# Kernel optimization log

Hardware: AMD Instinct MI355X
Metric: run time of the kernel (lower is better)

Reference implementation:

```python
import jax, jax.numpy as jnp
import numpy as np

S, T, B, IN, H, O = 64, 32, 512, 66, 1024, 1024  # S == max_length


def _gru_cell(x, h, Wih, Whh, bih, bhh):
    # PyTorch GRU cell: gates ordered (r, z, n)
    gi = x @ Wih.T + bih            # [B, 3H]
    gh = h @ Whh.T + bhh            # [B, 3H]
    ir, iz, inn = jnp.split(gi, 3, axis=1)
    hr, hz, hn = jnp.split(gh, 3, axis=1)
    r = jax.nn.sigmoid(ir + hr)
    z = jax.nn.sigmoid(iz + hz)
    n = jnp.tanh(inn + r * hn)
    return (1.0 - z) * n + z * h


def setup_inputs() -> dict:
    key = jax.random.key(0)
    ks = jax.random.split(key, 20)
    s = 0.02
    return {
        "input_tensor": jax.random.normal(ks[0], (S, B, IN), jnp.float32),
        "target_tensor": jax.random.normal(ks[1], (T, B, H), jnp.float32),
        # encoder GRU
        "enc_Wih": jax.random.normal(ks[2], (3 * H, IN), jnp.float32) * s,
        "enc_Whh": jax.random.normal(ks[3], (3 * H, H), jnp.float32) * s,
        "enc_bih": jax.random.normal(ks[4], (3 * H,), jnp.float32) * s,
        "enc_bhh": jax.random.normal(ks[5], (3 * H,), jnp.float32) * s,
        # attention: Linear(2H -> max_length)
        "attn_W": jax.random.normal(ks[6], (S, 2 * H), jnp.float32) * s,
        "attn_b": jax.random.normal(ks[7], (S,), jnp.float32) * s,
        # attn_combine: Linear(2H -> H)
        "comb_W": jax.random.normal(ks[8], (H, 2 * H), jnp.float32) * s,
        "comb_b": jax.random.normal(ks[9], (H,), jnp.float32) * s,
        # decoder GRU
        "dec_Wih": jax.random.normal(ks[10], (3 * H, H), jnp.float32) * s,
        "dec_Whh": jax.random.normal(ks[11], (3 * H, H), jnp.float32) * s,
        "dec_bih": jax.random.normal(ks[12], (3 * H,), jnp.float32) * s,
        "dec_bhh": jax.random.normal(ks[13], (3 * H,), jnp.float32) * s,
        # output: Linear(H -> O)
        "out_W": jax.random.normal(ks[14], (O, H), jnp.float32) * s,
        "out_b": jax.random.normal(ks[15], (O,), jnp.float32) * s,
    }


def reference(input_tensor, target_tensor, enc_Wih, enc_Whh, enc_bih, enc_bhh,
              attn_W, attn_b, comb_W, comb_b, dec_Wih, dec_Whh, dec_bih,
              dec_bhh, out_W, out_b):
    batch = input_tensor.shape[1]
    h0 = jnp.zeros((batch, enc_Whh.shape[1]), input_tensor.dtype)

    # ---- encoder GRU over time ----
    def enc_step(h, x):
        h2 = _gru_cell(x, h, enc_Wih, enc_Whh, enc_bih, enc_bhh)
        return h2, h2

    enc_h, enc_out = jax.lax.scan(enc_step, h0, input_tensor)  # enc_out: [S, B, H]

    # ---- attention decoder, teacher forcing; loop t = 1..T-1 uses target[t-1] ----
    def dec_step(h, x):
        aw = jax.nn.softmax(jnp.concatenate([x, h], axis=1) @ attn_W.T + attn_b,
                            axis=1)                              # [B, S]
        ctx = jnp.einsum('bl,lbh->bh', aw, enc_out)              # [B, H]
        comb = jax.nn.relu(jnp.concatenate([x, ctx], axis=1) @ comb_W.T + comb_b)
        h2 = _gru_cell(comb, h, dec_Wih, dec_Whh, dec_bih, dec_bhh)
        out = jax.nn.log_softmax(h2 @ out_W.T + out_b, axis=1)   # [B, O]
        return h2, out

    _, outs = jax.lax.scan(dec_step, enc_h, target_tensor[:-1])
    # original overwrites `outputs` every step -> only last step survives
    return outs[-1]
```

## Files before the change

### kernel.cpp

```cpp
#include <hip/hip_runtime.h>
#include <hip/hip_bf16.h>
#include <math.h>

#define S_LEN 64
#define T_LEN 32
#define BATCH 512
#define IN_DIM 66
#define INP 128
#define H_DIM 1024
#define O_DIM 1024
#define H3 3072

typedef __attribute__((ext_vector_type(8))) short short8;
typedef __attribute__((ext_vector_type(4))) float f32x4;
typedef __attribute__((ext_vector_type(4))) unsigned short us4;

__device__ __forceinline__ unsigned short f2b(float f) {
    union { float f; unsigned u; } x; x.f = f;
    unsigned r = x.u + 0x7FFF + ((x.u >> 16) & 1);
    return (unsigned short)(r >> 16);
}
__device__ __forceinline__ float b2f(unsigned short s) {
    union { unsigned u; float f; } x; x.u = ((unsigned)s) << 16;
    return x.f;
}
__device__ __forceinline__ void gll16(const void* g, const void* l) {
    __builtin_amdgcn_global_load_lds(
        (const __attribute__((address_space(1))) unsigned int*)g,
        (__attribute__((address_space(3))) unsigned int*)l, 16, 0, 0);
}

template<int TM, int TN>
__global__ __launch_bounds__(256) void gemm_k(
    const unsigned short* __restrict__ A, int lda,
    const unsigned short* __restrict__ W, int ldw,
    const float* __restrict__ bias,
    const float* __restrict__ addf, const unsigned short* __restrict__ addb,
    int ldadd,
    float* __restrict__ Cf,
    unsigned short* __restrict__ Cb, int ldc,
    int K, int flags)
{
    constexpr int IF = TM / 16;
    constexpr int JF = TN / 64;
    constexpr int NW = TN / 4;
    constexpr int CA = TM * 4;
    constexpr int CW = TN * 4;
    __shared__ __align__(16) unsigned short As[2][TM * 32];
    __shared__ __align__(16) unsigned short Bs[2][TN * 32];

    const int bm = blockIdx.y * TM;
    const int bn = blockIdx.x * TN;
    const int t = threadIdx.x;
    const int lane = t & 63;
    const int wv = t >> 6;
    const int ln = lane & 15;
    const int quad = lane >> 4;

    f32x4 acc[IF][JF];
    #pragma unroll
    for (int i = 0; i < IF; i++)
        #pragma unroll
// ... 41 lines not shown
            af[ii] = *(const short8*)&As[cur][(ii * 16 + ln) * 32 + quad * 8];
        #pragma unroll
        for (int j = 0; j < JF; j++)
            bf[j] = *(const short8*)&Bs[cur][(wv * NW + j * 16 + ln) * 32 + quad * 8];
        #pragma unroll
        for (int ii = 0; ii < IF; ii++)
            #pragma unroll
            for (int j = 0; j < JF; j++)
                acc[ii][j] = __builtin_amdgcn_mfma_f32_16x16x32_bf16(
                    af[ii], bf[j], acc[ii][j], 0, 0, 0);
        __syncthreads();
    }

    #pragma unroll
    for (int i = 0; i < IF; i++) {
        #pragma unroll
        for (int j = 0; j < JF; j++) {
            #pragma unroll
            for (int r = 0; r < 4; r++) {
                int m = bm + i * 16 + quad * 4 + r;
                int n = bn + wv * NW + j * 16 + ln;
                float v = acc[i][j][r];
                if (flags & 1) v += bias[n];
                if (flags & 2) v += addf[(size_t)m * ldadd + n];
                if (flags & 4) v += b2f(addb[(size_t)m * ldadd + n]);
                if (flags & 8) v = fmaxf(v, 0.f);
                if (flags & 16) Cf[(size_t)m * ldc + n] = v;
                if (flags & 32) Cb[(size_t)m * ldc + n] = f2b(v);
            }
        }
    }
}

__device__ __forceinline__ void gru_stage(
    const unsigned short* __restrict__ A, int lda,
    const unsigned short* __restrict__ W, int ldw, int kb,
    unsigned short* As_g, unsigned short* Ws_g,
    int bm, int bn, int gt, int gwv)
{
    {
        int s = gt >> 7, r = (gt >> 2) & 31, c = gt & 3;
        gll16(A + (size_t)(bm + r) * lda + kb + s * 32 + c * 8,
              (const char*)As_g + gwv * 1024);
    }
    #pragma unroll
    for (int j = 0; j < 6; j++) {
        int ch = j * 256 + gt;
        int g2 = ch >> 9, ch2 = ch & 511;
        int s = ch2 >> 8, r = (ch2 >> 2) & 63, c = ch2 & 3;
        gll16(W + (size_t)(g2 * H_DIM + bn + r) * ldw + kb + s * 32 + c * 8,
              (const char*)Ws_g + j * 4096 + gwv * 1024);
    }
}

__device__ __forceinline__ void gru_compute(
    const unsigned short* As_g, const unsigned short* Ws_g,
    int gwv, int ln, int quad,
    f32x4 (&accR)[2], f32x4 (&accZ)[2], f32x4 (&accN)[2])
{
    #pragma unroll
    for (int sub = 0; sub < 2; sub++) {
        short8 a[2], bw[3];
        #pragma unroll
        for (int i = 0; i < 2; i++)
            a[i] = *(const short8*)&As_g[sub * 1024 + (i * 16 + ln) * 32 + quad * 8];
        #pragma unroll
        for (int g = 0; g < 3; g++)
            bw[g] = *(const short8*)&Ws_g[g * 4096 + sub * 2048 + (gwv * 16 + ln) * 32 + quad * 8];
        #pragma unroll
        for (int i = 0; i < 2; i++) {
            accR[i] = __builtin_amdgcn_mfma_f32_16x16x32_bf16(a[i], bw[0], accR[i], 0, 0, 0);
            accZ[i] = __builtin_amdgcn_mfma_f32_16x16x32_bf16(a[i], bw[1], accZ[i], 0, 0, 0);
            accN[i] = __builtin_amdgcn_mfma_f32_16x16x32_bf16(a[i], bw[2], accN[i], 0, 0, 0);
        }
    }
}

__global__ __launch_bounds__(512) void gru_gemm(
    const unsigned short* __restrict__ A0, int lda0,
    const unsigned short* __restrict__ W0, int ldw0, int K0,
    const unsigned short* __restrict__ A1,
    const unsigned short* __restrict__ W1,
    const float* __restrict__ bih, const float* __restrict__ bhh,
    const float* __restrict__ hf_in, float* __restrict__ hf_out,
    unsigned short* __restrict__ hb_out, unsigned short* __restrict__ slot)
{
    __shared__ __align__(16) unsigned short As2[2][2][2 * 32 * 32];
    __shared__ __align__(16) unsigned short Ws2[2][2][3 * 2 * 64 * 32];
    const int bm = blockIdx.y * 32;
    const int bn = blockIdx.x * 64;
    const int t = threadIdx.x;
    const int wg = t >> 8;
    const int gt = t & 255;
    const int lane = t & 63;
    const int gwv = gt >> 6;
    const int ln = lane & 15;
    const int quad = lane >> 4;

    f32x4 accR[2], accZ[2], accN0[2], accN1[2];
    #pragma unroll
    for (int i = 0; i < 2; i++) {
        f32x4 z = {0.f, 0.f, 0.f, 0.f};
        accR[i] = z; accZ[i] = z; accN0[i] = z; accN1[i] = z;
    }

    const int half0 = K0 >> 1;
    const int nt0 = half0 >> 6;
    const int nt = nt0 + 8;

    auto stg = [&](int i, int buf) {
        const unsigned short* A; int lda; const unsigned short* W; int ldw; int kb;
        if (i < nt0) { A = A0; lda = lda0; W = W0; ldw = ldw0; kb = wg * half0 + (i << 6); }
        else         { A = A1; lda = H_DIM; W = W1; ldw = H_DIM; kb = wg * 512 + ((i - nt0) << 6); }
        gru_stage(A, lda, W, ldw, kb, As2[wg][buf], Ws2[wg][buf], bm, bn, gt, gwv);
    };

    stg(0, 0);
    __syncthreads();
    for (int i = 0; i < nt; ++i) {
        const int cur = i & 1;
        if (i + 1 < nt) stg(i + 1, cur ^ 1);
        if (i < nt0)
            gru_compute(As2[wg][cur], Ws2[wg][cur], gwv, ln, quad, accR, accZ, accN0);
        else
            gru_compute(As2[wg][cur], Ws2[wg][cur], gwv, ln, quad, accR, accZ, accN1);
        __syncthreads();
    }

    float* red = (float*)Ws2;
    const int rb = (gwv * 64 + lane) * 33;
    if (wg == 1) {
        #pragma unroll
        for (int i = 0; i < 2; i++)
            #pragma unroll
            for (int r = 0; r < 4; r++) {
                red[rb + i * 4 + r]      = accR[i][r];
                red[rb + 8 + i * 4 + r]  = accZ[i][r];
                red[rb + 16 + i * 4 + r] = accN0[i][r];
                red[rb + 24 + i * 4 + r] = accN1[i][r];
            }
    }
    __syncthreads();
    if (wg == 0) {
        #pragma unroll
        for (int i = 0; i < 2; i++)
            #pragma unroll
            for (int r = 0; r < 4; r++) {
                accR[i][r]  += red[rb + i * 4 + r];
                accZ[i][r]  += red[rb + 8 + i * 4 + r];
                accN0[i][r] += red[rb + 16 + i * 4 + r];
                accN1[i][r] += red[rb + 24 + i * 4 + r];
            }
        const int n = bn + gwv * 16 + ln;
        const float br = bih[n] + bhh[n];
        const float bz = bih[H_DIM + n] + bhh[H_DIM + n];
        const float bi_n = bih[2 * H_DIM + n];
        const float bh_n = bhh[2 * H_DIM + n];
        #pragma unroll
        for (int i = 0; i < 2; i++) {
            #pragma unroll
            for (int r = 0; r < 4; r++) {
                const int m = bm + i * 16 + quad * 4 + r;
                const size_t idx = (size_t)m * H_DIM + n;
                float rg = 1.f / (1.f + __expf(-(accR[i][r] + br)));
                float zg = 1.f / (1.f + __expf(-(accZ[i][r] + bz)));
                float av = accN0[i][r] + bi_n + rg * (accN1[i][r] + bh_n);
                float e2 = __expf(-2.f * fabsf(av));
                float th = (1.f - e2) / (1.f + e2);
                th = av < 0.f ? -th : th;
                float o = (1.f - zg) * th + zg * hf_in[idx];
                hf_out[idx] = o;
                unsigned short ob = f2b(o);
                hb_out[idx] = ob;
                if (slot) slot[idx] = ob;
            }
        }
    }
}

__global__ __launch_bounds__(256) void attn_ctx(
    const unsigned short* __restrict__ hb,
    const unsigned short* __restrict__ wAhT,
    const unsigned short* __restrict__ attnx_t,
    const unsigned short* __restrict__ encb,
    unsigned short* __restrict__ ctx)
{
    __shared__ float hf[H_DIM];
    __shared__ float part[4][S_LEN];
    __shared__ float awl[S_LEN];
    const int b = blockIdx.x, t = threadIdx.x;
    {
        us4 u = *(const us4*)(hb + ((size_t)b << 10) + t * 4);
        #pragma unroll
        for (int j = 0; j < 4; j++) hf[t * 4 + j] = b2f(u[j]);
    }
    __syncthreads();
    {
        const int c = t & 63, ks = (t >> 6) * 256;
        float s = 0.f;
        #pragma unroll 8
        for (int k = 0; k < 256; k++)
            s += hf[ks + k] * b2f(wAhT[(size_t)(ks + k) * S_LEN + c]);
        part[t >> 6][c] = s;
    }
    __syncthreads();
    if (t < 64) {
        float v = part[0][t] + part[1][t] + part[2][t] + part[3][t]
                + b2f(attnx_t[b * S_LEN + t]);
        float m = v;
        #pragma unroll
        for (int off = 32; off; off >>= 1) m = fmaxf(m, __shfl_xor(m, off));
        float e = __expf(v - m);
        float ss = e;
        #pragma unroll
        for (int off = 32; off; off >>= 1) ss += __shfl_xor(ss, off);
        awl[t] = e / ss;
    }
    __syncthreads();
    const int hq = t * 4;
    float s0 = 0.f, s1 = 0.f, s2 = 0.f, s3 = 0.f;
    #pragma unroll 4
    for (int l = 0; l < S_LEN; l++) {
        us4 u = *(const us4*)(encb + (((size_t)l * BATCH + b) << 10) + hq);
        float w = awl[l];
        s0 += w * b2f(u[0]); s1 += w * b2f(u[1]);
        s2 += w * b2f(u[2]); s3 += w * b2f(u[3]);
    }
    us4 o; o[0] = f2b(s0); o[1] = f2b(s1); o[2] = f2b(s2); o[3] = f2b(s3);
    *(us4*)(ctx + ((size_t)b << 10) + hq) = o;
}

__global__ void cvt_w4(const float* __restrict__ src, int ld,
                       unsigned short* __restrict__ dst, int rows, int cols)
{
    int idx = blockIdx.x * blockDim.x + threadIdx.x;
    int total4 = rows * cols / 4;
    if (idx >= total4) return;
    int e = idx * 4;
    int r = e / cols, c = e - r * cols;
    const float* s = src + (size_t)r * ld + c;
    us4 o;
    #pragma unroll
    for (int j = 0; j < 4; j++) o[j] = f2b(s[j]);
    *(us4*)(dst + e) = o;
}

__global__ void cvt_plain4(const float* __restrict__ src,
                           unsigned short* __restrict__ dst, int total4)
{
    int idx = blockIdx.x * blockDim.x + threadIdx.x;
    if (idx >= total4) return;
    f32x4 v = *(const f32x4*)(src + (size_t)idx * 4);
    us4 o;
    #pragma unroll
    for (int j = 0; j < 4; j++) o[j] = f2b(v[j]);
    *(us4*)(dst + (size_t)idx * 4) = o;
}

__global__ void cvt_pad(const float* __restrict__ src, int scols,
                        unsigned short* __restrict__ dst, int dcols, int total)
{
    int idx = blockIdx.x * blockDim.x + threadIdx.x;
    if (idx >= total) return;
    int r = idx / dcols, c = idx - r * dcols;
    dst[idx] = (c < scols) ? f2b(src[(size_t)r * scols + c]) : (unsigned short)0;
}

__global__ void cvt_attT(const float* __restrict__ attn_W,
                         unsigned short* __restrict__ dst)
{
    int idx = blockIdx.x * blockDim.x + threadIdx.x;
    if (idx >= S_LEN * H_DIM) return;
    int k = idx >> 6, c = idx & 63;
    dst[idx] = f2b(attn_W[(size_t)c * 2 * H_DIM + H_DIM + k]);
}

__global__ void log_softmax1024(float* __restrict__ x)
{
    __shared__ float red[256];
    float* xr = x + (size_t)blockIdx.x * O_DIM;
    int t = threadIdx.x;
    float m = -1e30f;
    for (int i = t; i < O_DIM; i += 256) m = fmaxf(m, xr[i]);
    red[t] = m; __syncthreads();
    for (int s2 = 128; s2 > 0; s2 >>= 1) {
        if (t < s2) red[t] = fmaxf(red[t], red[t + s2]);
        __syncthreads();
    }
    m = red[0];
    __syncthreads();
    float s = 0.f;
    for (int i = t; i < O_DIM; i += 256) s += expf(xr[i] - m);
    red[t] = s; __syncthreads();
    for (int s2 = 128; s2 > 0; s2 >>= 1) {
        if (t < s2) red[t] += red[t + s2];
        __syncthreads();
    }
    float lse = m + logf(red[0]);
    __syncthreads();
    for (int i = t; i < O_DIM; i += 256) xr[i] = xr[i] - lse;
}

extern "C" void kernel_launch(void* const* d_in, const int* in_sizes, int n_in,
                              void* d_out, int out_size, void* d_ws, size_t ws_size,
                              hipStream_t stream)
{
    const float* input   = (const float*)d_in[0];
// ... 6 lines not shown
    const float* attn_b  = (const float*)d_in[7];
    const float* comb_W  = (const float*)d_in[8];
    const float* comb_b  = (const float*)d_in[9];
    const float* dec_Wih = (const float*)d_in[10];
    const float* dec_Whh = (const float*)d_in[11];
    const float* dec_bih = (const float*)d_in[12];
    const float* dec_bhh = (const float*)d_in[13];
    const float* out_W   = (const float*)d_in[14];
    const float* out_b   = (const float*)d_in[15];
    float* out = (float*)d_out;

    char* p = (char*)d_ws;
    auto alloc = [&](size_t bytes) {
        char* r = p; p += (bytes + 255) & ~(size_t)255; return r;
    };
    unsigned short* wWhh  = (unsigned short*)alloc((size_t)H3 * H_DIM * 2);
    unsigned short* wDih  = (unsigned short*)alloc((size_t)H3 * H_DIM * 2);
    unsigned short* wDhh  = (unsigned short*)alloc((size_t)H3 * H_DIM * 2);
    unsigned short* wCc   = (unsigned short*)alloc((size_t)H_DIM * H_DIM * 2);
    unsigned short* wCx   = (unsigned short*)alloc((size_t)H_DIM * H_DIM * 2);
    unsigned short* wO    = (unsigned short*)alloc((size_t)O_DIM * H_DIM * 2);
    unsigned short* wAhT  = (unsigned short*)alloc((size_t)H_DIM * S_LEN * 2);
    unsigned short* wAx   = (unsigned short*)alloc((size_t)S_LEN * H_DIM * 2);
    unsigned short* wIhp  = (unsigned short*)alloc((size_t)H3 * INP * 2);
    unsigned short* xbp   = (unsigned short*)alloc((size_t)S_LEN * BATCH * INP * 2);
    unsigned short* encb  = (unsigned short*)alloc((size_t)S_LEN * BATCH * H_DIM * 2);
    unsigned short* combx = (unsigned short*)alloc((size_t)(T_LEN - 1) * BATCH * H_DIM * 2);
    unsigned short* attnx = (unsigned short*)alloc((size_t)(T_LEN - 1) * BATCH * S_LEN * 2);
    float*          h     = (float*)alloc((size_t)BATCH * H_DIM * 4);
    unsigned short* hbA   = (unsigned short*)alloc((size_t)BATCH * H_DIM * 2);
    unsigned short* hbB   = (unsigned short*)alloc((size_t)BATCH * H_DIM * 2);
    unsigned short* ctx   = (unsigned short*)alloc((size_t)BATCH * H_DIM * 2);
    unsigned short* comb  = (unsigned short*)alloc((size_t)BATCH * H_DIM * 2);
    unsigned short* targetb = encb;

    const dim3 blk(256);

    hipMemsetAsync(h,   0, (size_t)BATCH * H_DIM * 4, stream);
    hipMemsetAsync(hbA, 0, (size_t)BATCH * H_DIM * 2, stream);

    cvt_w4<<<(H3 * H_DIM / 4 + 255) / 256, blk, 0, stream>>>(enc_Whh, H_DIM, wWhh, H3, H_DIM);
    cvt_w4<<<(H3 * H_DIM / 4 + 255) / 256, blk, 0, stream>>>(dec_Wih, H_DIM, wDih, H3, H_DIM);
    cvt_w4<<<(H3 * H_DIM / 4 + 255) / 256, blk, 0, stream>>>(dec_Whh, H_DIM, wDhh, H3, H_DIM);
    cvt_w4<<<(H_DIM * H_DIM / 4 + 255) / 256, blk, 0, stream>>>(comb_W + H_DIM, 2 * H_DIM, wCc, H_DIM, H_DIM);
    cvt_w4<<<(H_DIM * H_DIM / 4 + 255) / 256, blk, 0, stream>>>(comb_W, 2 * H_DIM, wCx, H_DIM, H_DIM);
    cvt_w4<<<(O_DIM * H_DIM / 4 + 255) / 256, blk, 0, stream>>>(out_W, H_DIM, wO, O_DIM, H_DIM);
    cvt_w4<<<(S_LEN * H_DIM / 4 + 255) / 256, blk, 0, stream>>>(attn_W, 2 * H_DIM, wAx, S_LEN, H_DIM);
    cvt_attT<<<(S_LEN * H_DIM + 255) / 256, blk, 0, stream>>>(attn_W, wAhT);
    cvt_pad<<<((S_LEN * BATCH * INP) + 255) / 256, blk, 0, stream>>>(
        input, IN_DIM, xbp, INP, S_LEN * BATCH * INP);
    cvt_pad<<<((H3 * INP) + 255) / 256, blk, 0, stream>>>(
        enc_Wih, IN_DIM, wIhp, INP, H3 * INP);
    cvt_plain4<<<((T_LEN * BATCH * H_DIM / 4) + 255) / 256, blk, 0, stream>>>(
        target, targetb, T_LEN * BATCH * H_DIM / 4);

    const int MT = (T_LEN - 1) * BATCH;
    gemm_k<64, 64><<<dim3(1, MT / 64), blk, 0, stream>>>(
        targetb, H_DIM, wAx, H_DIM, attn_b,
        nullptr, nullptr, 0, nullptr, attnx, S_LEN, H_DIM, 1 | 32);
    gemm_k<128, 128><<<dim3(H_DIM / 128, MT / 128), blk, 0, stream>>>(
        targetb, H_DIM, wCx, H_DIM, comb_b,
        nullptr, nullptr, 0, nullptr, combx, H_DIM, H_DIM, 1 | 32);

    const dim3 grid_gru(H_DIM / 64, BATCH / 32);
    const dim3 blk512(512);
    unsigned short* hcur = hbA;
    unsigned short* hnxt = hbB;

    for (int s = 0; s < S_LEN; s++) {
        gru_gemm<<<grid_gru, blk512, 0, stream>>>(
            xbp + (size_t)s * BATCH * INP, INP, wIhp, INP, INP,
            hcur, wWhh, enc_bih, enc_bhh, h, h, hnxt,
            encb + (size_t)s * BATCH * H_DIM);
        unsigned short* tmp = hcur; hcur = hnxt; hnxt = tmp;
    }

    for (int t = 0; t < T_LEN - 1; t++) {
        attn_ctx<<<BATCH, blk, 0, stream>>>(
            hcur, wAhT, attnx + (size_t)t * BATCH * S_LEN, encb, ctx);
        gemm_k<32, 64><<<dim3(H_DIM / 64, BATCH / 32), blk, 0, stream>>>(
            ctx, H_DIM, wCc, H_DIM, nullptr,
            nullptr, combx + (size_t)t * BATCH * H_DIM, H_DIM,
            nullptr, comb, H_DIM, H_DIM, 4 | 8 | 32);
        gru_gemm<<<grid_gru, blk512, 0, stream>>>(
            comb, H_DIM, wDih, H_DIM, H_DIM,
            hcur, wDhh, dec_bih, dec_bhh, h, h, hnxt, nullptr);
        unsigned short* tmp = hcur; hcur = hnxt; hnxt = tmp;
    }

    gemm_k<32, 64><<<dim3(O_DIM / 64, BATCH / 32), blk, 0, stream>>>(
        hcur, H_DIM, wO, H_DIM, out_b,
        nullptr, nullptr, 0, out, nullptr, O_DIM, H_DIM, 1 | 16);
    log_softmax1024<<<BATCH, blk, 0, stream>>>(out);
}
```

Measured before the change: 3.089 ms.

## Replace per-step GRU launches with persistent encoder/decoder kernels using grid barriers

The per-timestep kernel launches for the encoder GRU and the decoder steps (attention, combine, GRU) become two persistent kernels of 256 blocks that loop over time and synchronise with atomic grid-wide barriers. The encoder overlaps the input projection for the next step with the barrier wait, and blocks are mapped so that neighbouring column tiles share an XCD. This removes about 150 kernel launches and their gaps. In exchange it relies on all 256 blocks being co-resident, since otherwise the spin barriers deadlock, and it pays for atomic spin-waits on every step.

After: 9.204 ms. 198% more time.

```diff
diff --git a/kernel.cpp b/kernel.cpp
--- a/kernel.cpp
+++ b/kernel.cpp
@@ -10,6 +10,7 @@
 #define H_DIM 1024
 #define O_DIM 1024
 #define H3 3072
+#define NB 256
 
 typedef __attribute__((ext_vector_type(8))) short short8;
 typedef __attribute__((ext_vector_type(4))) float f32x4;
@@ -28,6 +29,24 @@
     __builtin_amdgcn_global_load_lds(
         (const __attribute__((address_space(1))) unsigned int*)g,
         (__attribute__((address_space(3))) unsigned int*)l, 16, 0, 0);
+}
+
+__device__ __forceinline__ void gbar_arrive(unsigned* bar) {
+    __threadfence();
+    __hip_atomic_fetch_add(bar, 1u, __ATOMIC_RELEASE, __HIP_MEMORY_SCOPE_AGENT);
+}
+__device__ __forceinline__ void gbar_wait(unsigned* bar, unsigned target) {
+    while (__hip_atomic_load(bar, __ATOMIC_RELAXED, __HIP_MEMORY_SCOPE_AGENT) < target)
+        __builtin_amdgcn_s_sleep(1);
+    __threadfence();
+}
+__device__ __forceinline__ void gsync(unsigned* bar, unsigned target) {
+    __syncthreads();
+    if (threadIdx.x == 0) {
+        gbar_arrive(bar);
+        gbar_wait(bar, target);
+    }
+    __syncthreads();
 }
 
 template<int TM, int TN>
@@ -135,7 +154,7 @@
     }
 }
 
-__device__ __forceinline__ void gru_stage(
+__device__ __forceinline__ void stage3(
     const unsigned short* __restrict__ A, int lda,
     const unsigned short* __restrict__ W, int ldw, int kb,
     unsigned short* As_g, unsigned short* Ws_g,
@@ -156,7 +175,27 @@
     }
 }
 
-__device__ __forceinline__ void gru_compute(
+__device__ __forceinline__ void stage1(
+    const unsigned short* __restrict__ A, int lda,
+    const unsigned short* __restrict__ W, int ldw, int kb,
+    unsigned short* As_g, unsigned short* Ws_g,
+    int bm, int bn, int gt, int gwv)
+{
+    {
+        int s = gt >> 7, r = (gt >> 2) & 31, c = gt & 3;
+        gll16(A + (size_t)(bm + r) * lda + kb + s * 32 + c * 8,
+              (const char*)As_g + gwv * 1024);
+    }
+    #pragma unroll
+    for (int j = 0; j < 2; j++) {
+        int ch = j * 256 + gt;
+        int s = ch >> 8, r = (ch >> 2) & 63, c = ch & 3;
+        gll16(W + (size_t)(bn + r) * ldw + kb + s * 32 + c * 8,
+              (const char*)Ws_g + j * 4096 + gwv * 1024);
+    }
+}
+
+__device__ __forceinline__ void compute3(
     const unsigned short* As_g, const unsigned short* Ws_g,
     int gwv, int ln, int quad,
     f32x4 (&accR)[2], f32x4 (&accZ)[2], f32x4 (&accN)[2])
@@ -179,58 +218,30 @@
     }
 }
 
-__global__ __launch_bounds__(512) void gru_gemm(
-    const unsigned short* __restrict__ A0, int lda0,
-    const unsigned short* __restrict__ W0, int ldw0, int K0,
-    const unsigned short* __restrict__ A1,
-    const unsigned short* __restrict__ W1,
+__device__ __forceinline__ void compute1(
+    const unsigned short* As_g, const unsigned short* Ws_g,
+    int gwv, int ln, int quad, f32x4 (&accC)[2])
+{
+    #pragma unroll
+    for (int sub = 0; sub < 2; sub++) {
+        short8 a[2], bw;
+        #pragma unroll
+        for (int i = 0; i < 2; i++)
+            a[i] = *(const short8*)&As_g[sub * 1024 + (i * 16 + ln) * 32 + quad * 8];
+        bw = *(const short8*)&Ws_g[sub * 2048 + (gwv * 16 + ln) * 32 + quad * 8];
+        #pragma unroll
+        for (int i = 0; i < 2; i++)
+            accC[i] = __builtin_amdgcn_mfma_f32_16x16x32_bf16(a[i], bw, accC[i], 0, 0, 0);
+    }
+}
+
+__device__ __forceinline__ void gru_finish(
+    f32x4 (&accR)[2], f32x4 (&accZ)[2], f32x4 (&accN0)[2], f32x4 (&accN1)[2],
+    float* red, int wg, int gwv, int lane, int ln, int quad, int bm, int bn,
     const float* __restrict__ bih, const float* __restrict__ bhh,
-    const float* __restrict__ hf_in, float* __restrict__ hf_out,
+    float* __restrict__ h,
     unsigned short* __restrict__ hb_out, unsigned short* __restrict__ slot)
 {
-    __shared__ __align__(16) unsigned short As2[2][2][2 * 32 * 32];
-    __shared__ __align__(16) unsigned short Ws2[2][2][3 * 2 * 64 * 32];
-    const int bm = blockIdx.y * 32;
-    const int bn = blockIdx.x * 64;
-    const int t = threadIdx.x;
-    const int wg = t >> 8;
-    const int gt = t & 255;
-    const int lane = t & 63;
-    const int gwv = gt >> 6;
-    const int ln = lane & 15;
-    const int quad = lane >> 4;
-
-    f32x4 accR[2], accZ[2], accN0[2], accN1[2];
-    #pragma unroll
-    for (int i = 0; i < 2; i++) {
-        f32x4 z = {0.f, 0.f, 0.f, 0.f};
-        accR[i] = z; accZ[i] = z; accN0[i] = z; accN1[i] = z;
-    }
-
-    const int half0 = K0 >> 1;
-    const int nt0 = half0 >> 6;
-    const int nt = nt0 + 8;
-
-    auto stg = [&](int i, int buf) {
-        const unsigned short* A; int lda; const unsigned short* W; int ldw; int kb;
-        if (i < nt0) { A = A0; lda = lda0; W = W0; ldw = ldw0; kb = wg * half0 + (i << 6); }
-        else         { A = A1; lda = H_DIM; W = W1; ldw = H_DIM; kb = wg * 512 + ((i - nt0) << 6); }
-        gru_stage(A, lda, W, ldw, kb, As2[wg][buf], Ws2[wg][buf], bm, bn, gt, gwv);
-    };
-
-    stg(0, 0);
-    __syncthreads();
-    for (int i = 0; i < nt; ++i) {
-        const int cur = i & 1;
-        if (i + 1 < nt) stg(i + 1, cur ^ 1);
-        if (i < nt0)
-            gru_compute(As2[wg][cur], Ws2[wg][cur], gwv, ln, quad, accR, accZ, accN0);
-        else
-            gru_compute(As2[wg][cur], Ws2[wg][cur], gwv, ln, quad, accR, accZ, accN1);
-        __syncthreads();
-    }
-
-    float* red = (float*)Ws2;
     const int rb = (gwv * 64 + lane) * 33;
     if (wg == 1) {
         #pragma unroll
@@ -271,8 +282,8 @@
                 float e2 = __expf(-2.f * fabsf(av));
                 float th = (1.f - e2) / (1.f + e2);
                 th = av < 0.f ? -th : th;
-                float o = (1.f - zg) * th + zg * hf_in[idx];
-                hf_out[idx] = o;
+                float o = (1.f - zg) * th + zg * h[idx];
+                h[idx] = o;
                 unsigned short ob = f2b(o);
                 hb_out[idx] = ob;
                 if (slot) slot[idx] = ob;
@@ -281,56 +292,223 @@
     }
 }
 
-__global__ __launch_bounds__(256) void attn_ctx(
-    const unsigned short* __restrict__ hb,
+__global__ __launch_bounds__(512) void enc_persist(
+    const unsigned short* __restrict__ xbp,
+    const unsigned short* __restrict__ wIhp,
+    const unsigned short* __restrict__ wWhh,
+    const float* __restrict__ bih, const float* __restrict__ bhh,
+    float* __restrict__ h,
+    unsigned short* __restrict__ hb0,
+    unsigned short* __restrict__ hb1,
+    unsigned short* __restrict__ encb,
+    unsigned* __restrict__ bar)
+{
+    __shared__ __align__(16) unsigned short As2[2][2][2048];
+    __shared__ __align__(16) unsigned short Ws2[2][2][12288];
+
+    const int bid = blockIdx.x;
+    const int xcd = bid & 7, sb = bid >> 3;
+    const int bn = (xcd * 2 + (sb >> 4)) * 64;
+    const int bm = (sb & 15) * 32;
+    const int t = threadIdx.x;
+    const int wg = t >> 8;
+    const int gt = t & 255;
+    const int lane = t & 63;
+    const int gwv = gt >> 6;
+    const int ln = lane & 15;
+    const int quad = lane >> 4;
+
+    unsigned short* hb[2] = {hb0, hb1};
+
+    for (int s = 0; s < S_LEN; ++s) {
+        f32x4 accR[2], accZ[2], accN0[2], accN1[2];
+        #pragma unroll
+        for (int i = 0; i < 2; i++) {
+            f32x4 z = {0.f, 0.f, 0.f, 0.f};
+            accR[i] = z; accZ[i] = z; accN0[i] = z; accN1[i] = z;
+        }
+        stage3(xbp + (size_t)s * BATCH * INP, INP, wIhp, INP, wg * 64,
+               As2[wg][0], Ws2[wg][0], bm, bn, gt, gwv);
+        __syncthreads();
+        compute3(As2[wg][0], Ws2[wg][0], gwv, ln, quad, accR, accZ, accN0);
+        if (t == 0 && s > 0) gbar_wait(bar, (unsigned)(s * NB));
+        __syncthreads();
+        const unsigned short* A1 = hb[s & 1];
+        stage3(A1, H_DIM, wWhh, H_DIM, wg * 512, As2[wg][1], Ws2[wg][1],
+               bm, bn, gt, gwv);
+        __syncthreads();
+        for (int i = 0; i < 8; ++i) {
+            const int cur = (i + 1) & 1;
+            if (i + 1 < 8)
+                stage3(A1, H_DIM, wWhh, H_DIM, wg * 512 + ((i + 1) << 6),
+                       As2[wg][cur ^ 1], Ws2[wg][cur ^ 1], bm, bn, gt, gwv);
+            compute3(As2[wg][cur], Ws2[wg][cur], gwv, ln, quad, accR, accZ, accN1);
+            __syncthreads();
+        }
+        gru_finish(accR, accZ, accN0, accN1, (float*)Ws2, wg, gwv, lane, ln,
+                   quad, bm, bn, bih, bhh, h, hb[(s + 1) & 1],
+                   encb + (size_t)s * BATCH * H_DIM);
+        __syncthreads();
+        if (t == 0 && s < S_LEN - 1) gbar_arrive(bar);
+    }
+}
+
+__global__ __launch_bounds__(512) void dec_persist(
     const unsigned short* __restrict__ wAhT,
-    const unsigned short* __restrict__ attnx_t,
+    const unsigned short* __restrict__ attnx,
     const unsigned short* __restrict__ encb,
-    unsigned short* __restrict__ ctx)
-{
-    __shared__ float hf[H_DIM];
-    __shared__ float part[4][S_LEN];
-    __shared__ float awl[S_LEN];
-    const int b = blockIdx.x, t = threadIdx.x;
-    {
-        us4 u = *(const us4*)(hb + ((size_t)b << 10) + t * 4);
-        #pragma unroll
-        for (int j = 0; j < 4; j++) hf[t * 4 + j] = b2f(u[j]);
-    }
-    __syncthreads();
-    {
-        const int c = t & 63, ks = (t >> 6) * 256;
-        float s = 0.f;
-        #pragma unroll 8
-        for (int k = 0; k < 256; k++)
-            s += hf[ks + k] * b2f(wAhT[(size_t)(ks + k) * S_LEN + c]);
-        part[t >> 6][c] = s;
-    }
-    __syncthreads();
-    if (t < 64) {
-        float v = part[0][t] + part[1][t] + part[2][t] + part[3][t]
-                + b2f(attnx_t[b * S_LEN + t]);
-        float m = v;
-        #pragma unroll
-        for (int off = 32; off; off >>= 1) m = fmaxf(m, __shfl_xor(m, off));
-        float e = __expf(v - m);
-        float ss = e;
-        #pragma unroll
-        for (int off = 32; off; off >>= 1) ss += __shfl_xor(ss, off);
-        awl[t] = e / ss;
-    }
-    __syncthreads();
-    const int hq = t * 4;
-    float s0 = 0.f, s1 = 0.f, s2 = 0.f, s3 = 0.f;
-    #pragma unroll 4
-    for (int l = 0; l < S_LEN; l++) {
-        us4 u = *(const us4*)(encb + (((size_t)l * BATCH + b) << 10) + hq);
-        float w = awl[l];
-        s0 += w * b2f(u[0]); s1 += w * b2f(u[1]);
-        s2 += w * b2f(u[2]); s3 += w * b2f(u[3]);
-    }
-    us4 o; o[0] = f2b(s0); o[1] = f2b(s1); o[2] = f2b(s2); o[3] = f2b(s3);
-    *(us4*)(ctx + ((size_t)b << 10) + hq) = o;
+    const unsigned short* __restrict__ combx,
+    const unsigned short* __restrict__ wCc,
+    const unsigned short* __restrict__ wDih,
+    const unsigned short* __restrict__ wDhh,
+    const float* __restrict__ bih, const float* __restrict__ bhh,
+    float* __restrict__ h,
+    unsigned short* __restrict__ hb0, unsigned short* __restrict__ hb1,
+    unsigned short* __restrict__ ctx, unsigned short* __restrict__ comb,
+    unsigned* __restrict__ bar)
+{
+    __shared__ __align__(16) unsigned short As2[2][2][2048];
+    __shared__ __align__(16) unsigned short Ws2[2][2][12288];
+    float* hfs  = (float*)Ws2;
+    float* part = hfs + 2048;
+    float* awl  = part + 512;
+
+    const int bid = blockIdx.x;
+    const int xcd = bid & 7, sb = bid >> 3;
+    const int bn = (xcd * 2 + (sb >> 4)) * 64;
+    const int bm = (sb & 15) * 32;
+    const int t = threadIdx.x;
+    const int wg = t >> 8;
+    const int gt = t & 255;
+    const int lane = t & 63;
+    const int gwv = gt >> 6;
+    const int ln = lane & 15;
+    const int quad = lane >> 4;
+
+    unsigned short* hb[2] = {hb0, hb1};
+    unsigned tgt = 0;
+
+    for (int td = 0; td < T_LEN - 1; ++td) {
+        const unsigned short* hc = hb[td & 1];
+        {
+            const int tt = t & 255, r2 = t >> 8;
+            const int b = bid * 2 + r2;
+            {
+                us4 u = *(const us4*)(hc + ((size_t)b << 10) + tt * 4);
+                #pragma unroll
+                for (int j = 0; j < 4; j++) hfs[r2 * 1024 + tt * 4 + j] = b2f(u[j]);
+            }
+            __syncthreads();
+            {
+                const int c = tt & 63, ks = (tt >> 6) * 256;
+                float sc = 0.f;
+                #pragma unroll 8
+                for (int k = 0; k < 256; k++)
+                    sc += hfs[r2 * 1024 + ks + k] * b2f(wAhT[(size_t)(ks + k) * S_LEN + c]);
+                part[(r2 * 4 + (tt >> 6)) * 64 + c] = sc;
+            }
+            __syncthreads();
+            if (tt < 64) {
+                float v = part[r2 * 256 + tt] + part[r2 * 256 + 64 + tt]
+                        + part[r2 * 256 + 128 + tt] + part[r2 * 256 + 192 + tt]
+                        + b2f(attnx[((size_t)td * BATCH + b) * S_LEN + tt]);
+                float m = v;
+                #pragma unroll
+                for (int off = 32; off; off >>= 1) m = fmaxf(m, __shfl_xor(m, off));
+                float e = __expf(v - m);
+                float ss = e;
+                #pragma unroll
+                for (int off = 32; off; off >>= 1) ss += __shfl_xor(ss, off);
+                awl[r2 * 64 + tt] = e / ss;
+            }
+            __syncthreads();
+            const int hq = tt * 4;
+            float s0 = 0.f, s1 = 0.f, s2 = 0.f, s3 = 0.f;
+            #pragma unroll 4
+            for (int l = 0; l < S_LEN; l++) {
+                us4 u = *(const us4*)(encb + (((size_t)l * BATCH + b) << 10) + hq);
+                float w = awl[r2 * 64 + l];
+                s0 += w * b2f(u[0]); s1 += w * b2f(u[1]);
+                s2 += w * b2f(u[2]); s3 += w * b2f(u[3]);
+            }
+            us4 o; o[0] = f2b(s0); o[1] = f2b(s1); o[2] = f2b(s2); o[3] = f2b(s3);
+            *(us4*)(ctx + ((size_t)b << 10) + hq) = o;
+        }
+        tgt += NB; gsync(bar, tgt);
+        {
+            f32x4 accC[2];
+            {
+                f32x4 z = {0.f, 0.f, 0.f, 0.f};
+                accC[0] = z; accC[1] = z;
+            }
+            stage1(ctx, H_DIM, wCc, H_DIM, wg * 512,
+                   As2[wg][0], Ws2[wg][0], bm, bn, gt, gwv);
+            __syncthreads();
+            for (int i = 0; i < 8; ++i) {
+                const int cur = i & 1;
+                if (i + 1 < 8)
+                    stage1(ctx, H_DIM, wCc, H_DIM, wg * 512 + ((i + 1) << 6),
+                           As2[wg][cur ^ 1], Ws2[wg][cur ^ 1], bm, bn, gt, gwv);
+                compute1(As2[wg][cur], Ws2[wg][cur], gwv, ln, quad, accC);
+                __syncthreads();
+            }
+            float* red = (float*)Ws2;
+            const int rb = (gwv * 64 + lane) * 33;
+            if (wg == 1) {
+                #pragma unroll
+                for (int i = 0; i < 2; i++)
+                    #pragma unroll
+                    for (int r = 0; r < 4; r++)
+                        red[rb + i * 4 + r] = accC[i][r];
+            }
+            __syncthreads();
+            if (wg == 0) {
+                const int n = bn + gwv * 16 + ln;
+                #pragma unroll
+                for (int i = 0; i < 2; i++) {
+                    #pragma unroll
+                    for (int r = 0; r < 4; r++) {
+                        const int m = bm + i * 16 + quad * 4 + r;
+                        float v = accC[i][r] + red[rb + i * 4 + r]
+                                + b2f(combx[(size_t)td * BATCH * H_DIM + (size_t)m * H_DIM + n]);
+                        v = fmaxf(v, 0.f);
+                        comb[(size_t)m * H_DIM + n] = f2b(v);
+                    }
+                }
+            }
+        }
+        tgt += NB; gsync(bar, tgt);
+        {
+            f32x4 accR[2], accZ[2], accN0[2], accN1[2];
+            #pragma unroll
+            for (int i = 0; i < 2; i++) {
+                f32x4 z = {0.f, 0.f, 0.f, 0.f};
+                accR[i] = z; accZ[i] = z; accN0[i] = z; accN1[i] = z;
+            }
+            auto stgd = [&](int i, int buf) {
+                if (i < 8)
+                    stage3(comb, H_DIM, wDih, H_DIM, wg * 512 + (i << 6),
+                           As2[wg][buf], Ws2[wg][buf], bm, bn, gt, gwv);
+                else
+                    stage3(hc, H_DIM, wDhh, H_DIM, wg * 512 + ((i - 8) << 6),
+                           As2[wg][buf], Ws2[wg][buf], bm, bn, gt, gwv);
+            };
+            stgd(0, 0);
+            __syncthreads();
+            for (int i = 0; i < 16; ++i) {
+                const int cur = i & 1;
+                if (i + 1 < 16) stgd(i + 1, cur ^ 1);
+                if (i < 8)
+                    compute3(As2[wg][cur], Ws2[wg][cur], gwv, ln, quad, accR, accZ, accN0);
+                else
+                    compute3(As2[wg][cur], Ws2[wg][cur], gwv, ln, quad, accR, accZ, accN1);
+                __syncthreads();
+            }
+            gru_finish(accR, accZ, accN0, accN1, (float*)Ws2, wg, gwv, lane, ln,
+                       quad, bm, bn, bih, bhh, h, hb[(td + 1) & 1], nullptr);
+        }
+        if (td < T_LEN - 2) { tgt += NB; gsync(bar, tgt); }
+    }
 }
 
 __global__ void cvt_w4(const float* __restrict__ src, int ld,
@@ -448,12 +626,14 @@
     unsigned short* hbB   = (unsigned short*)alloc((size_t)BATCH * H_DIM * 2);
     unsigned short* ctx   = (unsigned short*)alloc((size_t)BATCH * H_DIM * 2);
     unsigned short* comb  = (unsigned short*)alloc((size_t)BATCH * H_DIM * 2);
+    unsigned*       bar   = (unsigned*)alloc(512);
     unsigned short* targetb = encb;
 
     const dim3 blk(256);
 
     hipMemsetAsync(h,   0, (size_t)BATCH * H_DIM * 4, stream);
     hipMemsetAsync(hbA, 0, (size_t)BATCH * H_DIM * 2, stream);
+    hipMemsetAsync(bar, 0, 512, stream);
 
     cvt_w4<<<(H3 * H_DIM / 4 + 255) / 256, blk, 0, stream>>>(enc_Whh, H_DIM, wWhh, H3, H_DIM);
     cvt_w4<<<(H3 * H_DIM / 4 + 255) / 256, blk, 0, stream>>>(dec_Wih, H_DIM, wDih, H3, H_DIM);
@@ -478,34 +658,15 @@
         targetb, H_DIM, wCx, H_DIM, comb_b,
         nullptr, nullptr, 0, nullptr, combx, H_DIM, H_DIM, 1 | 32);
 
-    const dim3 grid_gru(H_DIM / 64, BATCH / 32);
-    const dim3 blk512(512);
-    unsigned short* hcur = hbA;
-    unsigned short* hnxt = hbB;
-
-    for (int s = 0; s < S_LEN; s++) {
-        gru_gemm<<<grid_gru, blk512, 0, stream>>>(
-            xbp + (size_t)s * BATCH * INP, INP, wIhp, INP, INP,
-            hcur, wWhh, enc_bih, enc_bhh, h, h, hnxt,
-            encb + (size_t)s * BATCH * H_DIM);
-        unsigned short* tmp = hcur; hcur = hnxt; hnxt = tmp;
-    }
-
-    for (int t = 0; t < T_LEN - 1; t++) {
-        attn_ctx<<<BATCH, blk, 0, stream>>>(
-            hcur, wAhT, attnx + (size_t)t * BATCH * S_LEN, encb, ctx);
-        gemm_k<32, 64><<<dim3(H_DIM / 64, BATCH / 32), blk, 0, stream>>>(
-            ctx, H_DIM, wCc, H_DIM, nullptr,
-            nullptr, combx + (size_t)t * BATCH * H_DIM, H_DIM,
-            nullptr, comb, H_DIM, H_DIM, 4 | 8 | 32);
-        gru_gemm<<<grid_gru, blk512, 0, stream>>>(
-            comb, H_DIM, wDih, H_DIM, H_DIM,
-            hcur, wDhh, dec_bih, dec_bhh, h, h, hnxt, nullptr);
-        unsigned short* tmp = hcur; hcur = hnxt; hnxt = tmp;
-    }
+    enc_persist<<<NB, 512, 0, stream>>>(
+        xbp, wIhp, wWhh, enc_bih, enc_bhh, h, hbA, hbB, encb, bar);
+
+    dec_persist<<<NB, 512, 0, stream>>>(
+        wAhT, attnx, encb, combx, wCc, wDih, wDhh, dec_bih, dec_bhh,
+        h, hbA, hbB, ctx, comb, bar + 64);
 
     gemm_k<32, 64><<<dim3(O_DIM / 64, BATCH / 32), blk, 0, stream>>>(
-        hcur, H_DIM, wO, H_DIM, out_b,
+        hbB, H_DIM, wO, H_DIM, out_b,
         nullptr, nullptr, 0, out, nullptr, O_DIM, H_DIM, 1 | 16);
     log_softmax1024<<<BATCH, blk, 0, stream>>>(out);
 }
```

## Run encoder GRU as persistent kernel with global barrier; fuse conversion kernels

Applied to the files above, without the earlier changes.

Replaces the 64 per-step encoder GRU launches with one persistent kernel of 256 blocks that syncs between timesteps through an atomic counter barrier. Hidden-state stores and loads use cache-bypassing sc bits so other blocks see fresh data. It also remaps block indices for XCD-aware tiling in gru_gemm and merges the eleven conversion kernels into one grid-stride kernel. This cuts launch overhead and tail gaps, but risks deadlock if not all 256 blocks are co-resident, and adds barrier spin cost each step.

New measurement: 3.104 ms. No clear change (+0.5%).

```diff
diff --git a/kernel.cpp b/kernel.cpp
--- a/kernel.cpp
+++ b/kernel.cpp
@@ -10,6 +10,8 @@
 #define H_DIM 1024
 #define O_DIM 1024
 #define H3 3072
+#define NB 256
+#define AUX_SC 17
 
 typedef __attribute__((ext_vector_type(8))) short short8;
 typedef __attribute__((ext_vector_type(4))) float f32x4;
@@ -24,10 +26,25 @@
     union { unsigned u; float f; } x; x.u = ((unsigned)s) << 16;
     return x.f;
 }
-__device__ __forceinline__ void gll16(const void* g, const void* l) {
+template<int AUX>
+__device__ __forceinline__ void gll16x(const void* g, const void* l) {
     __builtin_amdgcn_global_load_lds(
         (const __attribute__((address_space(1))) unsigned int*)g,
-        (__attribute__((address_space(3))) unsigned int*)l, 16, 0, 0);
+        (__attribute__((address_space(3))) unsigned int*)l, 16, 0, AUX);
+}
+__device__ __forceinline__ void gll16(const void* g, const void* l) {
+    gll16x<0>(g, l);
+}
+__device__ __forceinline__ void store_b16_sc(unsigned short* p, unsigned v) {
+    asm volatile("global_store_short %0, %1, off sc0 sc1" :: "v"(p), "v"(v) : "memory");
+}
+
+__device__ __forceinline__ void gbar_arrive(unsigned* bar) {
+    __hip_atomic_fetch_add(bar, 1u, __ATOMIC_RELAXED, __HIP_MEMORY_SCOPE_AGENT);
+}
+__device__ __forceinline__ void gbar_wait(unsigned* bar, unsigned target) {
+    while (__hip_atomic_load(bar, __ATOMIC_RELAXED, __HIP_MEMORY_SCOPE_AGENT) < target)
+        __builtin_amdgcn_s_sleep(2);
 }
 
 template<int TM, int TN>
@@ -135,6 +152,7 @@
     }
 }
 
+template<int AAUX>
 __device__ __forceinline__ void gru_stage(
     const unsigned short* __restrict__ A, int lda,
     const unsigned short* __restrict__ W, int ldw, int kb,
@@ -143,8 +161,8 @@
 {
     {
         int s = gt >> 7, r = (gt >> 2) & 31, c = gt & 3;
-        gll16(A + (size_t)(bm + r) * lda + kb + s * 32 + c * 8,
-              (const char*)As_g + gwv * 1024);
+        gll16x<AAUX>(A + (size_t)(bm + r) * lda + kb + s * 32 + c * 8,
+                     (const char*)As_g + gwv * 1024);
     }
     #pragma unroll
     for (int j = 0; j < 6; j++) {
@@ -179,58 +197,14 @@
     }
 }
 
-__global__ __launch_bounds__(512) void gru_gemm(
-    const unsigned short* __restrict__ A0, int lda0,
-    const unsigned short* __restrict__ W0, int ldw0, int K0,
-    const unsigned short* __restrict__ A1,
-    const unsigned short* __restrict__ W1,
+template<bool SC>
+__device__ __forceinline__ void gru_finish(
+    f32x4 (&accR)[2], f32x4 (&accZ)[2], f32x4 (&accN0)[2], f32x4 (&accN1)[2],
+    float* red, int wg, int gwv, int lane, int ln, int quad, int bm, int bn,
     const float* __restrict__ bih, const float* __restrict__ bhh,
     const float* __restrict__ hf_in, float* __restrict__ hf_out,
     unsigned short* __restrict__ hb_out, unsigned short* __restrict__ slot)
 {
-    __shared__ __align__(16) unsigned short As2[2][2][2 * 32 * 32];
-    __shared__ __align__(16) unsigned short Ws2[2][2][3 * 2 * 64 * 32];
-    const int bm = blockIdx.y * 32;
-    const int bn = blockIdx.x * 64;
-    const int t = threadIdx.x;
-    const int wg = t >> 8;
-    const int gt = t & 255;
-    const int lane = t & 63;
-    const int gwv = gt >> 6;
-    const int ln = lane & 15;
-    const int quad = lane >> 4;
-
-    f32x4 accR[2], accZ[2], accN0[2], accN1[2];
-    #pragma unroll
-    for (int i = 0; i < 2; i++) {
-        f32x4 z = {0.f, 0.f, 0.f, 0.f};
-        accR[i] = z; accZ[i] = z; accN0[i] = z; accN1[i] = z;
-    }
-
-    const int half0 = K0 >> 1;
-    const int nt0 = half0 >> 6;
-    const int nt = nt0 + 8;
-
-    auto stg = [&](int i, int buf) {
-        const unsigned short* A; int lda; const unsigned short* W; int ldw; int kb;
-        if (i < nt0) { A = A0; lda = lda0; W = W0; ldw = ldw0; kb = wg * half0 + (i << 6); }
-        else         { A = A1; lda = H_DIM; W = W1; ldw = H_DIM; kb = wg * 512 + ((i - nt0) << 6); }
-        gru_stage(A, lda, W, ldw, kb, As2[wg][buf], Ws2[wg][buf], bm, bn, gt, gwv);
-    };
-
-    stg(0, 0);
-    __syncthreads();
-    for (int i = 0; i < nt; ++i) {
-        const int cur = i & 1;
-        if (i + 1 < nt) stg(i + 1, cur ^ 1);
-        if (i < nt0)
-            gru_compute(As2[wg][cur], Ws2[wg][cur], gwv, ln, quad, accR, accZ, accN0);
-        else
-            gru_compute(As2[wg][cur], Ws2[wg][cur], gwv, ln, quad, accR, accZ, accN1);
-        __syncthreads();
-    }
-
-    float* red = (float*)Ws2;
     const int rb = (gwv * 64 + lane) * 33;
     if (wg == 1) {
         #pragma unroll
@@ -274,11 +248,130 @@
                 float o = (1.f - zg) * th + zg * hf_in[idx];
                 hf_out[idx] = o;
                 unsigned short ob = f2b(o);
-                hb_out[idx] = ob;
+                if (SC) store_b16_sc(hb_out + idx, (unsigned)ob);
+                else    hb_out[idx] = ob;
                 if (slot) slot[idx] = ob;
             }
         }
     }
+}
+
+__global__ __launch_bounds__(512) void enc_persist(
+    const unsigned short* __restrict__ xbp,
+    const unsigned short* __restrict__ wIhp,
+    const unsigned short* __restrict__ wWhh,
+    const float* __restrict__ bih, const float* __restrict__ bhh,
+    float* __restrict__ h,
+    unsigned short* __restrict__ hb0,
+    unsigned short* __restrict__ hb1,
+    unsigned short* __restrict__ encb,
+    unsigned* __restrict__ bar)
+{
+    __shared__ __align__(16) unsigned short As2[2][2][2048];
+    __shared__ __align__(16) unsigned short Ws2[2][2][12288];
+
+    const int bid = blockIdx.x;
+    const int xcd = bid & 7, sb = bid >> 3;
+    const int bn = (xcd * 2 + (sb >> 4)) * 64;
+    const int bm = (sb & 15) * 32;
+    const int t = threadIdx.x;
+    const int wg = t >> 8;
+    const int gt = t & 255;
+    const int lane = t & 63;
+    const int gwv = gt >> 6;
+    const int ln = lane & 15;
+    const int quad = lane >> 4;
+
+    unsigned short* hb[2] = {hb0, hb1};
+
+    for (int s = 0; s < S_LEN; ++s) {
+        f32x4 accR[2], accZ[2], accN0[2], accN1[2];
+        #pragma unroll
+        for (int i = 0; i < 2; i++) {
+            f32x4 z = {0.f, 0.f, 0.f, 0.f};
+            accR[i] = z; accZ[i] = z; accN0[i] = z; accN1[i] = z;
+        }
+        gru_stage<0>(xbp + (size_t)s * BATCH * INP, INP, wIhp, INP, wg * 64,
+                     As2[wg][0], Ws2[wg][0], bm, bn, gt, gwv);
+        __syncthreads();
+        gru_compute(As2[wg][0], Ws2[wg][0], gwv, ln, quad, accR, accZ, accN0);
+        if (t == 0 && s > 0) gbar_wait(bar, (unsigned)(s * NB));
+        __syncthreads();
+        const unsigned short* A1 = hb[s & 1];
+        gru_stage<AUX_SC>(A1, H_DIM, wWhh, H_DIM, wg * 512,
+                          As2[wg][1], Ws2[wg][1], bm, bn, gt, gwv);
+        __syncthreads();
+        for (int i = 0; i < 8; ++i) {
+            const int cur = (i + 1) & 1;
+            if (i + 1 < 8)
+                gru_stage<AUX_SC>(A1, H_DIM, wWhh, H_DIM, wg * 512 + ((i + 1) << 6),
+                                  As2[wg][cur ^ 1], Ws2[wg][cur ^ 1], bm, bn, gt, gwv);
+            gru_compute(As2[wg][cur], Ws2[wg][cur], gwv, ln, quad, accR, accZ, accN1);
+            __syncthreads();
+        }
+        gru_finish<true>(accR, accZ, accN0, accN1, (float*)Ws2, wg, gwv, lane,
+                         ln, quad, bm, bn, bih, bhh, h, h, hb[(s + 1) & 1],
+                         encb + (size_t)s * BATCH * H_DIM);
+        __syncthreads();
+        if (t == 0 && s < S_LEN - 1) gbar_arrive(bar);
+    }
+}
+
+__global__ __launch_bounds__(512) void gru_gemm(
+    const unsigned short* __restrict__ A0, int lda0,
+    const unsigned short* __restrict__ W0, int ldw0, int K0,
+    const unsigned short* __restrict__ A1,
+    const unsigned short* __restrict__ W1,
+    const float* __restrict__ bih, const float* __restrict__ bhh,
+    const float* __restrict__ hf_in, float* __restrict__ hf_out,
+    unsigned short* __restrict__ hb_out, unsigned short* __restrict__ slot)
+{
+    __shared__ __align__(16) unsigned short As2[2][2][2 * 32 * 32];
+    __shared__ __align__(16) unsigned short Ws2[2][2][3 * 2 * 64 * 32];
+    const int lin = blockIdx.y * gridDim.x + blockIdx.x;
+    const int xcd = lin & 7, j = lin >> 3;
+    const int bn = (xcd * 2 + (j & 1)) * 64;
+    const int bm = (j >> 1) * 32;
+    const int t = threadIdx.x;
+    const int wg = t >> 8;
+    const int gt = t & 255;
+    const int lane = t & 63;
+    const int gwv = gt >> 6;
+    const int ln = lane & 15;
+    const int quad = lane >> 4;
+
+    f32x4 accR[2], accZ[2], accN0[2], accN1[2];
+    #pragma unroll
+    for (int i = 0; i < 2; i++) {
+        f32x4 z = {0.f, 0.f, 0.f, 0.f};
+        accR[i] = z; accZ[i] = z; accN0[i] = z; accN1[i] = z;
+    }
+
+    const int half0 = K0 >> 1;
+    const int nt0 = half0 >> 6;
+    const int nt = nt0 + 8;
+
+    auto stg = [&](int i, int buf) {
+        const unsigned short* A; int lda; const unsigned short* W; int ldw; int kb;
+        if (i < nt0) { A = A0; lda = lda0; W = W0; ldw = ldw0; kb = wg * half0 + (i << 6); }
+        else         { A = A1; lda = H_DIM; W = W1; ldw = H_DIM; kb = wg * 512 + ((i - nt0) << 6); }
+        gru_stage<0>(A, lda, W, ldw, kb, As2[wg][buf], Ws2[wg][buf], bm, bn, gt, gwv);
+    };
+
+    stg(0, 0);
+    __syncthreads();
+    for (int i = 0; i < nt; ++i) {
+        const int cur = i & 1;
+        if (i + 1 < nt) stg(i + 1, cur ^ 1);
+        if (i < nt0)
+            gru_compute(As2[wg][cur], Ws2[wg][cur], gwv, ln, quad, accR, accZ, accN0);
+        else
+            gru_compute(As2[wg][cur], Ws2[wg][cur], gwv, ln, quad, accR, accZ, accN1);
+        __syncthreads();
+    }
+
+    gru_finish<false>(accR, accZ, accN0, accN1, (float*)Ws2, wg, gwv, lane,
+                      ln, quad, bm, bn, bih, bhh, hf_in, hf_out, hb_out, slot);
 }
 
 __global__ __launch_bounds__(256) void attn_ctx(
@@ -333,49 +426,77 @@
     *(us4*)(ctx + ((size_t)b << 10) + hq) = o;
 }
 
-__global__ void cvt_w4(const float* __restrict__ src, int ld,
-                       unsigned short* __restrict__ dst, int rows, int cols)
-{
-    int idx = blockIdx.x * blockDim.x + threadIdx.x;
-    int total4 = rows * cols / 4;
-    if (idx >= total4) return;
-    int e = idx * 4;
-    int r = e / cols, c = e - r * cols;
-    const float* s = src + (size_t)r * ld + c;
-    us4 o;
-    #pragma unroll
-    for (int j = 0; j < 4; j++) o[j] = f2b(s[j]);
-    *(us4*)(dst + e) = o;
-}
-
-__global__ void cvt_plain4(const float* __restrict__ src,
-                           unsigned short* __restrict__ dst, int total4)
-{
-    int idx = blockIdx.x * blockDim.x + threadIdx.x;
-    if (idx >= total4) return;
-    f32x4 v = *(const f32x4*)(src + (size_t)idx * 4);
-    us4 o;
-    #pragma unroll
-    for (int j = 0; j < 4; j++) o[j] = f2b(v[j]);
-    *(us4*)(dst + (size_t)idx * 4) = o;
-}
-
-__global__ void cvt_pad(const float* __restrict__ src, int scols,
-                        unsigned short* __restrict__ dst, int dcols, int total)
-{
-    int idx = blockIdx.x * blockDim.x + threadIdx.x;
-    if (idx >= total) return;
-    int r = idx / dcols, c = idx - r * dcols;
-    dst[idx] = (c < scols) ? f2b(src[(size_t)r * scols + c]) : (unsigned short)0;
-}
-
-__global__ void cvt_attT(const float* __restrict__ attn_W,
-                         unsigned short* __restrict__ dst)
-{
-    int idx = blockIdx.x * blockDim.x + threadIdx.x;
-    if (idx >= S_LEN * H_DIM) return;
-    int k = idx >> 6, c = idx & 63;
-    dst[idx] = f2b(attn_W[(size_t)c * 2 * H_DIM + H_DIM + k]);
+__global__ __launch_bounds__(256) void cvt_all(
+    const float* __restrict__ enc_Whh, const float* __restrict__ dec_Wih,
+    const float* __restrict__ dec_Whh, const float* __restrict__ comb_W,
+    const float* __restrict__ out_W,   const float* __restrict__ attn_W,
+    const float* __restrict__ enc_Wih, const float* __restrict__ input,
+    const float* __restrict__ target,
+    unsigned short* __restrict__ wWhh, unsigned short* __restrict__ wDih,
+    unsigned short* __restrict__ wDhh, unsigned short* __restrict__ wCc,
+    unsigned short* __restrict__ wCx,  unsigned short* __restrict__ wO,
+    unsigned short* __restrict__ wAx,  unsigned short* __restrict__ wAhT,
+    unsigned short* __restrict__ wIhp, unsigned short* __restrict__ xbp,
+    unsigned short* __restrict__ targetb)
+{
+    const unsigned nW = H3 * H_DIM / 4;
+    const unsigned nH = H_DIM * H_DIM / 4;
+    const unsigned nA = S_LEN * H_DIM / 4;
+    const unsigned nI = H3 * INP / 4;
+    const unsigned nX = S_LEN * BATCH * INP / 4;
+    const unsigned nT = T_LEN * BATCH * H_DIM / 4;
+    const unsigned total = 3 * nW + 3 * nH + 2 * nA + nI + nX + nT;
+
+    auto plain4 = [](const float* s, unsigned short* d, unsigned i) {
+        f32x4 v = *(const f32x4*)(s + (size_t)i * 4);
+        us4 o;
+        #pragma unroll
+        for (int j = 0; j < 4; j++) o[j] = f2b(v[j]);
+        *(us4*)(d + (size_t)i * 4) = o;
+    };
+    auto strided4 = [](const float* s, int ld, int off, int c4s,
+                       unsigned short* d, unsigned i) {
+        int r = i / c4s, c4 = i - r * c4s;
+        f32x4 v = *(const f32x4*)(s + (size_t)r * ld + off + c4 * 4);
+        us4 o;
+        #pragma unroll
+        for (int j = 0; j < 4; j++) o[j] = f2b(v[j]);
+        *(us4*)(d + (size_t)i * 4) = o;
+    };
+    auto pad4 = [](const float* s, unsigned short* d, unsigned i) {
+        int r = i >> 5, c = (i & 31) * 4;
+        us4 o;
+        #pragma unroll
+        for (int j = 0; j < 4; j++) {
+            int cc = c + j;
+            o[j] = (cc < IN_DIM) ? f2b(s[(size_t)r * IN_DIM + cc]) : (unsigned short)0;
+        }
+        *(us4*)(d + (size_t)r * INP + c) = o;
+    };
+
+    for (unsigned q = blockIdx.x * blockDim.x + threadIdx.x; q < total;
+         q += gridDim.x * blockDim.x) {
+        unsigned i = q;
+        if (i < nW) { plain4(enc_Whh, wWhh, i); continue; }  i -= nW;
+        if (i < nW) { plain4(dec_Wih, wDih, i); continue; }  i -= nW;
+        if (i < nW) { plain4(dec_Whh, wDhh, i); continue; }  i -= nW;
+        if (i < nH) { strided4(comb_W, 2 * H_DIM, H_DIM, H_DIM / 4, wCc, i); continue; }  i -= nH;
+        if (i < nH) { strided4(comb_W, 2 * H_DIM, 0, H_DIM / 4, wCx, i); continue; }  i -= nH;
+        if (i < nH) { plain4(out_W, wO, i); continue; }  i -= nH;
+        if (i < nA) { strided4(attn_W, 2 * H_DIM, 0, H_DIM / 4, wAx, i); continue; }  i -= nA;
+        if (i < nA) {
+            int idx = i * 4, k = idx >> 6, c = idx & 63;
+            us4 o;
+            #pragma unroll
+            for (int j = 0; j < 4; j++)
+                o[j] = f2b(attn_W[(size_t)(c + j) * 2 * H_DIM + H_DIM + k]);
+            *(us4*)(wAhT + idx) = o;
+            continue;
+        }  i -= nA;
+        if (i < nI) { pad4(enc_Wih, wIhp, i); continue; }  i -= nI;
+        if (i < nX) { pad4(input, xbp, i); continue; }  i -= nX;
+        plain4(target, targetb, i);
+    }
 }
 
 __global__ void log_softmax1024(float* __restrict__ x)
@@ -448,27 +569,18 @@
     unsigned short* hbB   = (unsigned short*)alloc((size_t)BATCH * H_DIM * 2);
     unsigned short* ctx   = (unsigned short*)alloc((size_t)BATCH * H_DIM * 2);
     unsigned short* comb  = (unsigned short*)alloc((size_t)BATCH * H_DIM * 2);
+    unsigned*       bar   = (unsigned*)alloc(512);
     unsigned short* targetb = encb;
 
     const dim3 blk(256);
 
     hipMemsetAsync(h,   0, (size_t)BATCH * H_DIM * 4, stream);
     hipMemsetAsync(hbA, 0, (size_t)BATCH * H_DIM * 2, stream);
-
-    cvt_w4<<<(H3 * H_DIM / 4 + 255) / 256, blk, 0, stream>>>(enc_Whh, H_DIM, wWhh, H3, H_DIM);
-    cvt_w4<<<(H3 * H_DIM / 4 + 255) / 256, blk, 0, stream>>>(dec_Wih, H_DIM, wDih, H3, H_DIM);
-    cvt_w4<<<(H3 * H_DIM / 4 + 255) / 256, blk, 0, stream>>>(dec_Whh, H_DIM, wDhh, H3, H_DIM);
-    cvt_w4<<<(H_DIM * H_DIM / 4 + 255) / 256, blk, 0, stream>>>(comb_W + H_DIM, 2 * H_DIM, wCc, H_DIM, H_DIM);
-    cvt_w4<<<(H_DIM * H_DIM / 4 + 255) / 256, blk, 0, stream>>>(comb_W, 2 * H_DIM, wCx, H_DIM, H_DIM);
-    cvt_w4<<<(O_DIM * H_DIM / 4 + 255) / 256, blk, 0, stream>>>(out_W, H_DIM, wO, O_DIM, H_DIM);
-    cvt_w4<<<(S_LEN * H_DIM / 4 + 255) / 256, blk, 0, stream>>>(attn_W, 2 * H_DIM, wAx, S_LEN, H_DIM);
-    cvt_attT<<<(S_LEN * H_DIM + 255) / 256, blk, 0, stream>>>(attn_W, wAhT);
-    cvt_pad<<<((S_LEN * BATCH * INP) + 255) / 256, blk, 0, stream>>>(
-        input, IN_DIM, xbp, INP, S_LEN * BATCH * INP);
-    cvt_pad<<<((H3 * INP) + 255) / 256, blk, 0, stream>>>(
-        enc_Wih, IN_DIM, wIhp, INP, H3 * INP);
-    cvt_plain4<<<((T_LEN * BATCH * H_DIM / 4) + 255) / 256, blk, 0, stream>>>(
-        target, targetb, T_LEN * BATCH * H_DIM / 4);
+    hipMemsetAsync(bar, 0, 512, stream);
+
+    cvt_all<<<2048, blk, 0, stream>>>(
+        enc_Whh, dec_Wih, dec_Whh, comb_W, out_W, attn_W, enc_Wih, input, target,
+        wWhh, wDih, wDhh, wCc, wCx, wO, wAx, wAhT, wIhp, xbp, targetb);
 
     const int MT = (T_LEN - 1) * BATCH;
     gemm_k<64, 64><<<dim3(1, MT / 64), blk, 0, stream>>>(
@@ -478,19 +590,13 @@
         targetb, H_DIM, wCx, H_DIM, comb_b,
         nullptr, nullptr, 0, nullptr, combx, H_DIM, H_DIM, 1 | 32);
 
+    enc_persist<<<NB, 512, 0, stream>>>(
+        xbp, wIhp, wWhh, enc_bih, enc_bhh, h, hbA, hbB, encb, bar);
+
     const dim3 grid_gru(H_DIM / 64, BATCH / 32);
     const dim3 blk512(512);
     unsigned short* hcur = hbA;
     unsigned short* hnxt = hbB;
-
-    for (int s = 0; s < S_LEN; s++) {
-        gru_gemm<<<grid_gru, blk512, 0, stream>>>(
-            xbp + (size_t)s * BATCH * INP, INP, wIhp, INP, INP,
-            hcur, wWhh, enc_bih, enc_bhh, h, h, hnxt,
-            encb + (size_t)s * BATCH * H_DIM);
-        unsigned short* tmp = hcur; hcur = hnxt; hnxt = tmp;
-    }
-
     for (int t = 0; t < T_LEN - 1; t++) {
         attn_ctx<<<BATCH, blk, 0, stream>>>(
             hcur, wAhT, attnx + (size_t)t * BATCH * S_LEN, encb, ctx);
```
